# Optimization experiments

Measured on AMD Instinct MI355X. Metric: run time of the kernel, lower is better.

The kernel has to match this reference:

```python
import jax, jax.numpy as jnp
from jax import lax
import numpy as np

TAU = 10.0      # tauSr == tauRef
THR = 1.0       # theta
WIDTH = 1.0     # tauRho (surrogate width)
SCALE = 1.0     # scaleRho (surrogate scale)
DECAY = float(np.exp(-1.0 / TAU))


@jax.custom_vjp
def _heaviside(v):
    # spike = 1[v >= theta]
    return (v >= THR).astype(v.dtype)

def _heaviside_fwd(v):
    return _heaviside(v), v

def _heaviside_bwd(v, g):
    # SLAYER exponential surrogate pdf: scaleRho/tauRho * exp(-|v-theta|/tauRho)
    return (g * (SCALE / WIDTH) * jnp.exp(-jnp.abs(v - THR) / WIDTH),)

_heaviside.defvjp(_heaviside_fwd, _heaviside_bwd)


def _conv2d(x, w, pad):
    # x: (B, Cin, H, W), w: (Cout, Cin, kh, kw); SLAYER convs have no bias
    return lax.conv_general_dilated(
        x, w, window_strides=(1, 1), padding=[(pad, pad), (pad, pad)],
        dimension_numbers=("NCHW", "OIHW", "NCHW"))


def _sumpool(x, k):
    # SLAYER pool = sum over kxk window (times a learned scalar applied outside)
    B, C, H, W = x.shape
    return x.reshape(B, C, H // k, k, W // k, k).sum(axis=(3, 5))


def _psp(seq):
    # exponential synaptic (PSP) filter along time: s[t] = a*s[t-1] + x[t]
    a = jnp.asarray(DECAY, seq.dtype)
    def step(s, x_t):
        s = a * s + x_t
        return s, s
    _, out = lax.scan(step, jnp.zeros_like(seq[0]), seq)
    return out  # (T, ...)


def _spikes(u):
    # thresholded spiking with decaying refractory feedback (scaleRef=1):
    # v[t] = u[t] - r[t]; s[t] = 1[v >= theta]; r[t+1] = b*(r[t] + theta*s[t])
    b = jnp.asarray(DECAY, u.dtype)
    def step(r, u_t):
        s = _heaviside(u_t - r)
        r_next = b * (r + THR * s)
        return r_next, s
    _, out = lax.scan(step, jnp.zeros_like(u[0]), u)
    return out  # (T, ...)


def _forward(x, conv1_w, conv2_w, lin_w, w_pool1, w_pool2):
    N, T, C, H, W = x.shape  # (64, 100, 2, 32, 32)
    h = _conv2d(x.reshape(N * T, C, H, W), conv1_w, 2)        # (NT, 4, 32, 32)
    h = _sumpool(h, 4) * w_pool1                               # (NT, 4, 8, 8)
    h = h.reshape(N, T, 4, 8, 8).swapaxes(0, 1)                # (T, N, 4, 8, 8)
    s1 = _spikes(_psp(h))                                      # (T, N, 4, 8, 8)
    h2 = _conv2d(s1.reshape(T * N, 4, 8, 8), conv2_w, 1)       # (TN, 8, 8, 8)
    h2 = (_sumpool(h2, 2) * w_pool2).reshape(T, N, 8, 4, 4)    # (T, N, 8, 4, 4)
    s2 = _spikes(_psp(h2))                                     # (T, N, 8, 4, 4)
    # dense = full-spatial conv (2, 8, 4, 4) -> (N, T, 2)
    return jnp.einsum("tnchw,ochw->nto", s2, lin_w)


def setup_inputs() -> dict:
    key = jax.random.key(0)
    ks = jax.random.split(key, 4)
    x = (jax.random.uniform(ks[0], (64, 100, 2, 32, 32)) < 0.1).astype(jnp.float32)
    conv1_w = jax.random.normal(ks[1], (4, 2, 5, 5), jnp.float32) * 0.3
    conv2_w = jax.random.normal(ks[2], (8, 4, 3, 3), jnp.float32) * 0.3
    lin_w = jax.random.normal(ks[3], (2, 8, 4, 4), jnp.float32) * 0.3
    w_pool1 = jnp.float32(1.0 / 16.0)  # 1.1*theta / (16 * 1.1)
    w_pool2 = jnp.float32(1.0 / 4.0)   # 1.1*theta / (4 * 1.1)
    return {"x": x, "conv1_w": conv1_w, "conv2_w": conv2_w, "lin_w": lin_w,
            "w_pool1": w_pool1, "w_pool2": w_pool2}


def reference(x, conv1_w, conv2_w, lin_w, w_pool1, w_pool2):
    return _forward(x, conv1_w, conv2_w, lin_w, w_pool1, w_pool2)
```

## Files before the change

kernel.cpp:

```cpp
#include <hip/hip_runtime.h>


#define DECAY 0.9048374180359595f

__global__ __launch_bounds__(128) void k0_fold(const float* __restrict__ w1,
        const float* __restrict__ w2, const float* __restrict__ wp1,
        const float* __restrict__ wp2, float* __restrict__ wl1,
        float* __restrict__ wl2) {
    const int tid = threadIdx.x;
    const float p1 = wp1[0], p2 = wp2[0];
    for (int idx = tid; idx < 512; idx += 128) {
        const int f = idx & 7, c = (idx >> 3) & 3, e = (idx >> 5) & 7, cin = idx >> 8;
        const int cc = c * 2 + cin;
        int alo = e - 3; if (alo < 0) alo = 0;
        int ahi = e;     if (ahi > 4) ahi = 4;
        int blo = f - 3; if (blo < 0) blo = 0;
        int bhi = f;     if (bhi > 4) bhi = 4;
        float s = 0.f;
        for (int a = alo; a <= ahi; ++a)
            for (int b = blo; b <= bhi; ++b)
                s += w1[cc * 25 + a * 5 + b];
        wl1[(cin * 8 + e) * 32 + c * 8 + f] = s * p1;
    }
    for (int idx = tid; idx < 512; idx += 128) {
        const int c2 = idx & 7, f = (idx >> 3) & 3, e = (idx >> 5) & 3, cin = idx >> 7;
        int alo = e - 1; if (alo < 0) alo = 0;
        int ahi = e;     if (ahi > 2) ahi = 2;
        int blo = f - 1; if (blo < 0) blo = 0;
        int bhi = f;     if (bhi > 2) bhi = 2;
        float s = 0.f;
        for (int aa = alo; aa <= ahi; ++aa)
            for (int bb = blo; bb <= bhi; ++bb)
                s += w2[((c2 * 4 + cin) * 3 + aa) * 3 + bb];
        wl2[c2 * 68 + cin * 16 + e * 4 + f] = s * p2;
    }
}

__global__ __launch_bounds__(64) void k1(const float* __restrict__ x,
        const float* __restrict__ wg, float* __restrict__ u1) {
    __shared__ __align__(16) float xs[2 * 1296];
    __shared__ __align__(16) float wl[512];
    const int lane = threadIdx.x;
    const int c = lane >> 4, i = (lane >> 1) & 7, jh = lane & 1;
    const int frame = blockIdx.x;
    const int n = frame / 100, t = frame % 100;

    *(float4*)(wl + 4 * lane)       = *(const float4*)(wg + 4 * lane);
    *(float4*)(wl + 256 + 4 * lane) = *(const float4*)(wg + 256 + 4 * lane);

    #pragma unroll
    for (int m0 = 0; m0 < 128; m0 += 64) {
        const int m = m0 + lane;
        if (m < 72) {
            const int cin = m / 36, rem = m % 36;
            const int rr = rem / 9, q4 = rem % 9;
            const int pr = (rr == 0) ? 0 : (rr == 1) ? 9 : (rr == 2) ? 26 : 35;
            *(float4*)(xs + cin * 1296 + pr * 36 + q4 * 4) = make_float4(0.f, 0.f, 0.f, 0.f);
        }
    }
    #pragma unroll
    for (int m0 = 0; m0 < 192; m0 += 64) {
        const int m = m0 + lane;
        if (m < 144) {
            const int cin = m / 72, rem = m % 72;
            const int side = rem & 1, pr = rem >> 1;
            *(float2*)(xs + cin * 1296 + pr * 36 + side * 34) = make_float2(0.f, 0.f);
        }
    }
    const float4* xg = (const float4*)(x + (size_t)frame * 2048);
    #pragma unroll
    for (int q = 0; q < 8; ++q) {
        const int m = q * 64 + lane;
        const float4 v = xg[m];
        const int li = 4 * m;
        const int cin = li >> 10, row = (li >> 5) & 31, col = li & 31;
        const int r = row + 2;
        const int pr = (r & 3) * 9 + (r >> 2);
        float* d = xs + cin * 1296 + pr * 36 + col + 2;
        *(float2*)(d)     = make_float2(v.x, v.y);
        *(float2*)(d + 2) = make_float2(v.z, v.w);
    }
    __syncthreads();

    float acc[4] = {0.f, 0.f, 0.f, 0.f};
    const float* tb = xs + i * 36 + jh * 16;
    #pragma unroll
    for (int cin = 0; cin < 2; ++cin) {
        #pragma unroll
        for (int e = 0; e < 8; ++e) {
            const int ro = cin * 1296 + ((e & 3) * 9 + (e >> 2)) * 36;
            float xr[20];
            #pragma unroll
            for (int b = 0; b < 5; ++b)
                *(float4*)(xr + 4 * b) = *(const float4*)(tb + ro + 4 * b);
            float wv[8];
            *(float4*)(wv)     = *(const float4*)(wl + (cin * 8 + e) * 32 + c * 8);
            *(float4*)(wv + 4) = *(const float4*)(wl + (cin * 8 + e) * 32 + c * 8 + 4);
            #pragma unroll
            for (int jj = 0; jj < 4; ++jj) {
                const int o = 4 * jj;
                acc[jj] += xr[o]*wv[0]   + xr[o+1]*wv[1] + xr[o+2]*wv[2]
                         + xr[o+3]*wv[3] + xr[o+4]*wv[4] + xr[o+5]*wv[5]
                         + xr[o+6]*wv[6] + xr[o+7]*wv[7];
            }
        }
    }
    *(float4*)(u1 + (size_t)t * 16384 + n * 256 + c * 64 + i * 8 + jh * 4) =
        make_float4(acc[0], acc[1], acc[2], acc[3]);
}

__global__ __launch_bounds__(64) void k2_scan(float* __restrict__ u) {
    const int id = blockIdx.x * 64 + threadIdx.x;
    const float a = DECAY;
    float* p = u + id;
    float v[100];
    #pragma unroll
    for (int k = 0; k < 100; ++k) v[k] = p[(size_t)k * 16384];
    float psp = 0.f, r = 0.f;
    #pragma unroll
    for (int k = 0; k < 100; ++k) {
        psp = a * psp + v[k];
        const float vv = psp - r;
        const float s = (vv >= 1.f) ? 1.f : 0.f;
        r = a * (r + s);
        p[(size_t)k * 16384] = s;
    }
}

__global__ __launch_bounds__(256) void k3(const float* __restrict__ s1,
        const float* __restrict__ wl2g, float* __restrict__ u2) {
    __shared__ __align__(16) float xs[8 * 660];
    __shared__ __align__(16) float wl[544];
    const int tid = threadIdx.x, sub = tid >> 5, l = tid & 31;

    for (int m = tid; m < 136; m += 256)
        *(float4*)(wl + 4 * m) = *(const float4*)(wl2g + 4 * m);

    float* xt = xs + sub * 660;
    float4* fz = (float4*)xt;
    for (int m = l; m < 160; m += 32) fz[m] = make_float4(0.f, 0.f, 0.f, 0.f);

    const int frame = blockIdx.x * 8 + sub;
    const int t = frame >> 6, n = frame & 63;
    const float* fr = s1 + (size_t)t * 16384 + n * 256;
    {
        const int cin = l >> 3, row = l & 7;
        const int r = row + 1;
        const int pr = (r & 1) * 5 + (r >> 1);
        const float4 v0 = *(const float4*)(fr + cin * 64 + row * 8);
        const float4 v1 = *(const float4*)(fr + cin * 64 + row * 8 + 4);
        *(float4*)(xt + cin * 160 + pr * 16 + 4) = v0;
        *(float4*)(xt + cin * 160 + pr * 16 + 8) = v1;
    }
    __syncthreads();

    const int c2 = l >> 2, i = l & 3;
    float acc[4] = {0.f, 0.f, 0.f, 0.f};
    const float* wb = wl + c2 * 68;
    const float* tb = xt + i * 16;
    #pragma unroll
    for (int cin = 0; cin < 4; ++cin) {
        #pragma unroll
        for (int e = 0; e < 4; ++e) {
            const int C = cin * 160 + ((e & 1) * 5 + (e >> 1)) * 16;
            float xr[16];
            #pragma unroll
            for (int b = 0; b < 4; ++b)
                *(float4*)(xr + 4 * b) = *(const float4*)(tb + C + 4 * b);
            float wv[4];
            *(float4*)(wv) = *(const float4*)(wb + cin * 16 + e * 4);
            #pragma unroll
            for (int j = 0; j < 4; ++j) {
                #pragma unroll
                for (int f = 0; f < 4; ++f)
                    acc[j] += xr[2 * j + f + 3] * wv[f];
            }
        }
    }
    *(float4*)(u2 + (size_t)t * 8192 + n * 128 + c2 * 16 + i * 4) =
        make_float4(acc[0], acc[1], acc[2], acc[3]);
}

__global__ __launch_bounds__(128, 2) void k45(const float* __restrict__ u2,
        const float* __restrict__ lw, float* __restrict__ out) {
    __shared__ float ls[25 * 128];
    const int f = threadIdx.x, n = blockIdx.x;
    const int wave = f >> 6, l = f & 63;
    const float a = DECAY;
    const float w0 = lw[l], w1v = lw[64 + l], w2v = lw[128 + l], w3v = lw[192 + l];
    float psp = 0.f, r = 0.f;
    const float* p = u2 + n * 128 + f;
    #pragma unroll 1
    for (int t0 = 0; t0 < 100; t0 += 25) {
        float v[25];
        #pragma unroll
        for (int k = 0; k < 25; ++k) v[k] = p[(size_t)(t0 + k) * 8192];
        #pragma unroll
        for (int k = 0; k < 25; ++k) {
            psp = a * psp + v[k];
            const float vv = psp - r;
            const float s = (vv >= 1.f) ? 1.f : 0.f;
            r = a * (r + s);
            ls[k * 128 + f] = s;
        }
        __syncthreads();
        const int base = wave ? 13 : 0, cnt = wave ? 12 : 13;
        for (int q = 0; q < cnt; ++q) {
            const int k = base + q;
            const float sa = ls[k * 128 + l], sb = ls[k * 128 + 64 + l];
            float a0 = sa * w0 + sb * w1v;
            float a1 = sa * w2v + sb * w3v;
            #pragma unroll
            for (int off = 32; off > 0; off >>= 1) {
                a0 += __shfl_down(a0, off);
                a1 += __shfl_down(a1, off);
            }
            if (l == 0) {
                const int tt = t0 + k;
                out[n * 200 + tt * 2]     = a0;
                out[n * 200 + tt * 2 + 1] = a1;
            }
        }
        __syncthreads();
    }
}

extern "C" void kernel_launch(void* const* d_in, const int* in_sizes, int n_in,
                              void* d_out, int out_size, void* d_ws, size_t ws_size,
                              hipStream_t stream) {
    const float* x   = (const float*)d_in[0];
    const float* w1  = (const float*)d_in[1];
    const float* w2  = (const float*)d_in[2];
    const float* lw  = (const float*)d_in[3];
    const float* wp1 = (const float*)d_in[4];
    const float* wp2 = (const float*)d_in[5];

    float* u1  = (float*)d_ws;
    float* u2  = u1 + 1638400;
    float* wl1 = u2 + 819200;
    float* wl2 = wl1 + 512;
    float* out = (float*)d_out;

    k0_fold<<<1, 128, 0, stream>>>(w1, w2, wp1, wp2, wl1, wl2);
    k1<<<6400, 64, 0, stream>>>(x, wl1, u1);
    k2_scan<<<256, 64, 0, stream>>>(u1);
    k3<<<800, 256, 0, stream>>>(u1, wl2, u2);
    k45<<<64, 128, 0, stream>>>(u2, lw, out);
}
```

Before: 143.6 us.

## Remap conv1 thread work to reuse input rows across two output channels

Each lane now computes two output channels over half of the eight row offsets instead of one channel over all eight. Each loaded row of input pixels is reused for two channels, roughly halving shared-memory input reads per lane. Partial sums are combined with a cross-lane shuffle, and a select picks which channel each lane stores. The cost is more accumulator registers plus the shuffle and select overhead.

```diff
diff --git a/kernel.cpp b/kernel.cpp
--- a/kernel.cpp
+++ b/kernel.cpp
@@ -41,7 +41,6 @@
     __shared__ __align__(16) float xs[2 * 1296];
     __shared__ __align__(16) float wl[512];
     const int lane = threadIdx.x;
-    const int c = lane >> 4, i = (lane >> 1) & 7, jh = lane & 1;
     const int frame = blockIdx.x;
     const int n = frame / 100, t = frame % 100;
 
@@ -82,31 +81,52 @@
     }
     __syncthreads();
 
-    float acc[4] = {0.f, 0.f, 0.f, 0.f};
-    const float* tb = xs + i * 36 + jh * 16;
+    const int cp = lane >> 5;
+    const int i  = (lane >> 2) & 7;
+    const int jh = (lane >> 1) & 1;
+    const int eh = lane & 1;
+
+    float acc[2][4] = {{0.f, 0.f, 0.f, 0.f}, {0.f, 0.f, 0.f, 0.f}};
+    const float* tb = xs + (i + eh) * 36 + jh * 16;
     #pragma unroll
     for (int cin = 0; cin < 2; ++cin) {
         #pragma unroll
-        for (int e = 0; e < 8; ++e) {
-            const int ro = cin * 1296 + ((e & 3) * 9 + (e >> 2)) * 36;
+        for (int et = 0; et < 4; ++et) {
+            const int ro = cin * 1296 + et * 9 * 36;
             float xr[20];
             #pragma unroll
             for (int b = 0; b < 5; ++b)
                 *(float4*)(xr + 4 * b) = *(const float4*)(tb + ro + 4 * b);
-            float wv[8];
-            *(float4*)(wv)     = *(const float4*)(wl + (cin * 8 + e) * 32 + c * 8);
-            *(float4*)(wv + 4) = *(const float4*)(wl + (cin * 8 + e) * 32 + c * 8 + 4);
-            #pragma unroll
-            for (int jj = 0; jj < 4; ++jj) {
-                const int o = 4 * jj;
-                acc[jj] += xr[o]*wv[0]   + xr[o+1]*wv[1] + xr[o+2]*wv[2]
-                         + xr[o+3]*wv[3] + xr[o+4]*wv[4] + xr[o+5]*wv[5]
-                         + xr[o+6]*wv[6] + xr[o+7]*wv[7];
-            }
-        }
-    }
-    *(float4*)(u1 + (size_t)t * 16384 + n * 256 + c * 64 + i * 8 + jh * 4) =
-        make_float4(acc[0], acc[1], acc[2], acc[3]);
+            float wv[16];
+            const float* wp = wl + (cin * 8 + eh * 4 + et) * 32 + cp * 16;
+            #pragma unroll
+            for (int q = 0; q < 4; ++q)
+                *(float4*)(wv + 4 * q) = *(const float4*)(wp + 4 * q);
+            #pragma unroll
+            for (int cl = 0; cl < 2; ++cl) {
+                #pragma unroll
+                for (int jj = 0; jj < 4; ++jj) {
+                    const int o = 4 * jj;
+                    acc[cl][jj] += xr[o]*wv[cl*8]     + xr[o+1]*wv[cl*8+1]
+                                 + xr[o+2]*wv[cl*8+2] + xr[o+3]*wv[cl*8+3]
+                                 + xr[o+4]*wv[cl*8+4] + xr[o+5]*wv[cl*8+5]
+                                 + xr[o+6]*wv[cl*8+6] + xr[o+7]*wv[cl*8+7];
+                }
+            }
+        }
+    }
+    #pragma unroll
+    for (int cl = 0; cl < 2; ++cl)
+        #pragma unroll
+        for (int jj = 0; jj < 4; ++jj)
+            acc[cl][jj] += __shfl_xor(acc[cl][jj], 1);
+
+    const float o0 = eh ? acc[1][0] : acc[0][0];
+    const float o1 = eh ? acc[1][1] : acc[0][1];
+    const float o2 = eh ? acc[1][2] : acc[0][2];
+    const float o3 = eh ? acc[1][3] : acc[0][3];
+    *(float4*)(u1 + (size_t)t * 16384 + n * 256 + (2 * cp + eh) * 64 + i * 8 + jh * 4) =
+        make_float4(o0, o1, o2, o3);
 }
 
 __global__ __launch_bounds__(64) void k2_scan(float* __restrict__ u) {
```

New measurement: 140.6 us. 2.1% less time.
